# Kernel tuning notes

Hardware: AMD Instinct MI355X
Metric: run time of the kernel (lower is better)

The kernel has to match this reference:

```python
import jax, jax.numpy as jnp
import numpy as np

B, T, D, E, TOP_K = 8, 2048, 512, 8, 2


def setup_inputs() -> dict:
    key = jax.random.key(0)
    ks = jax.random.split(key, 8)
    s = 0.02
    return {
        "x": jax.random.normal(ks[0], (B, T, D), dtype=jnp.float32),
        "eps": jax.random.normal(ks[1], (B, T, E), dtype=jnp.float32),
        "Wr": jax.random.normal(ks[2], (D, E), dtype=jnp.float32) * s,
        "br": jnp.zeros((E,), dtype=jnp.float32),
        "Wn": jax.random.normal(ks[3], (D, E), dtype=jnp.float32) * s,
        "bn": jnp.zeros((E,), dtype=jnp.float32),
        "Wk": jax.random.normal(ks[4], (E, D, D), dtype=jnp.float32) * s,
        "bk": jnp.zeros((E, D), dtype=jnp.float32),
    }


def reference(x, eps, Wr, br, Wn, bn, Wk, bk):
    # Noisy top-k router (NoisyTopkRouter.forward)
    logits = jnp.einsum("btd,de->bte", x, Wr) + br            # [B,T,E]
    noise_logits = jnp.einsum("btd,de->bte", x, Wn) + bn      # [B,T,E]
    noisy = logits + eps * jax.nn.softplus(noise_logits)      # [B,T,E]
    _, top_idx = jax.lax.top_k(noisy, TOP_K)                  # [B,T,k]
    # mask[b,t,e] = True iff expert e is in the token's top-k
    topk_mask = jax.nn.one_hot(top_idx, E, dtype=jnp.float32).sum(-2) > 0
    sparse_logits = jnp.where(topk_mask, noisy, -jnp.inf)
    gating = jax.nn.softmax(sparse_logits, axis=-1)           # zero for non-top-k experts
    # Dense dispatch: every expert's Linear applied to all tokens, then
    # gating (zero outside top-k) selects/scales — same math as the masked
    # gather + per-expert Linear + gating scale in SparseMoE.forward.
    expert_out = jnp.einsum("btd,edh->bteh", x, Wk) + bk      # [B,T,E,D]
    out = jnp.einsum("bte,bteh->bth", gating, expert_out)     # [B,T,D]
    return out
```

## Files before the change

kernel.cpp:

```cpp
#include <hip/hip_runtime.h>
#include <hip/hip_bf16.h>
#include <math.h>

#define B_    8
#define T_    2048
#define NTOK  (B_ * T_)
#define D_    512
#define E_    8
#define CAP   NTOK

#define RV_TOK    16
#define RV_THR    256
#define XS_STRIDE 132
#define WS_FLOATS 2108

typedef __attribute__((ext_vector_type(4))) float f32x4;
typedef __attribute__((ext_vector_type(8))) short short8;

__device__ __forceinline__ void async_load16(const void* g, void* l) {
    __builtin_amdgcn_global_load_lds(
        (const __attribute__((address_space(1))) unsigned int*)g,
        (__attribute__((address_space(3))) unsigned int*)l,
        16, 0, 0);
}

__global__ __launch_bounds__(256) void transpose_wk(
    const float* __restrict__ Wk, __hip_bfloat16* __restrict__ Wkt)
{
    __shared__ float tile[32][33];
    const int e  = blockIdx.z;
    const int d0 = blockIdx.x * 32;
    const int h0 = blockIdx.y * 32;
    const int tx = threadIdx.x, ty = threadIdx.y;

    const float* src = Wk + ((size_t)e * D_ + d0) * D_ + h0;
    #pragma unroll
    for (int r = ty; r < 32; r += 8)
        tile[r][tx] = src[(size_t)r * D_ + tx];
    __syncthreads();
    __hip_bfloat16* dst = Wkt + ((size_t)e * D_ + h0) * D_ + d0;
    #pragma unroll
    for (int r = ty; r < 32; r += 8)
        dst[(size_t)r * D_ + tx] = __float2bfloat16(tile[tx][r]);
}

__global__ __launch_bounds__(RV_THR) void router_kernel(
    const float* __restrict__ x,
    const float* __restrict__ eps,
    const float* __restrict__ Wr,
    const float* __restrict__ br,
    const float* __restrict__ Wn,
    const float* __restrict__ bn,
    __hip_bfloat16* __restrict__ xb,
    uint4* __restrict__ top2)
{
    __shared__ float xs[RV_TOK * XS_STRIDE];
    __shared__ float wsh[WS_FLOATS];

    const int tid  = threadIdx.x;
    const int tok0 = blockIdx.x * RV_TOK;
    const int lane = tid & 63, wv = tid >> 6;
    const int kidx = lane >> 2, ts = lane & 3;
    const int tl = wv * 4 + ts;
    const int wk = tid >> 1, wh = tid & 1;

    float acc[16];
    #pragma unroll
    for (int c = 0; c < 16; ++c) acc[c] = 0.f;

    for (int kc = 0; kc < D_; kc += 128) {
        #pragma unroll
        for (int it = 0; it < 2; ++it) {
            const int f   = it * RV_THR + tid;
            const int row = f >> 5, col = (f & 31) * 4;
            const f32x4 v = *(const f32x4*)(x + (size_t)(tok0 + row) * D_ + kc + col);
            *(f32x4*)(xs + row * XS_STRIDE + col) = v;
            union { __hip_bfloat16 h[4]; uint2 u; } cv;
            cv.h[0] = __float2bfloat16(v.x); cv.h[1] = __float2bfloat16(v.y);
            cv.h[2] = __float2bfloat16(v.z); cv.h[3] = __float2bfloat16(v.w);
            *(uint2*)(xb + (size_t)(tok0 + row) * D_ + kc + col) = cv.u;
        }
        {
            const float* src = (wh ? Wn : Wr) + (size_t)(kc + wk) * E_;
            const f32x4 w0 = *(const f32x4*)(src);
            const f32x4 w1 = *(const f32x4*)(src + 4);
            float* dst = wsh + wk * 16 + (wk >> 3) * 4 + wh * 8;
            *(f32x4*)(dst)     = w0;
            *(f32x4*)(dst + 4) = w1;
        }
        __syncthreads();

        const float* xra = xs + tl * XS_STRIDE + kidx * 8;
        const f32x4 xa0 = *(const f32x4*)(xra);
        const f32x4 xa1 = *(const f32x4*)(xra + 4);
        const float* wbase = wsh + kidx * 132;
        #pragma unroll
        for (int kk = 0; kk < 8; ++kk) {
            const float xav = (kk < 4) ? xa0[kk] : xa1[kk - 4];
            const float* wrow = wbase + kk * 16;
            #pragma unroll
            for (int c4 = 0; c4 < 4; ++c4) {
                const f32x4 w = *(const f32x4*)(wrow + c4 * 4);
                #pragma unroll
                for (int c = 0; c < 4; ++c)
                    acc[c4 * 4 + c] = fmaf(xav, w[c], acc[c4 * 4 + c]);
            }
        }
        __syncthreads();
    }

    #pragma unroll
    for (int off = 4; off < 64; off <<= 1) {
        #pragma unroll
        for (int c = 0; c < 16; ++c)
            acc[c] += __shfl_xor(acc[c], off);
    }

    if (lane < 4) {
        const int tok = tok0 + tl;
        float nv[8];
        #pragma unroll
        for (int e = 0; e < 8; ++e) {
            const float nl = acc[8 + e] + bn[e];
            const float sp = fmaxf(nl, 0.f) + log1pf(expf(-fabsf(nl)));
            nv[e] = acc[e] + br[e] + eps[(size_t)tok * E_ + e] * sp;
        }
        int i1 = 0; float v1 = nv[0];
        #pragma unroll
        for (int e = 1; e < 8; ++e)
            if (nv[e] > v1) { v1 = nv[e]; i1 = e; }
        int i2 = -1; float v2 = -3.4e38f;
        #pragma unroll
        for (int e = 0; e < 8; ++e)
            if (e != i1 && nv[e] > v2) { v2 = nv[e]; i2 = e; }
        const float t  = expf(v2 - v1);
        const float g1 = 1.f / (1.f + t);
        const float g2 = t / (1.f + t);
        top2[tok] = make_uint4((unsigned)i1 | ((unsigned)i2 << 8),
                               __float_as_uint(g1), __float_as_uint(g2), 0u);
    }
}

__global__ __launch_bounds__(256) void bucket_kernel(
    const uint4* __restrict__ top2,
    int* __restrict__ counts,
    uint2* __restrict__ entries)
{
    __shared__ int hist[E_];
    __shared__ int base[E_];
    const int tid = threadIdx.x;
    const int tok = blockIdx.x * 256 + tid;
    if (tid < E_) hist[tid] = 0;
    __syncthreads();
    const uint4 t = top2[tok];
    const int i1 = t.x & 0xff, i2 = (t.x >> 8) & 0xff;
    const int l1 = atomicAdd(&hist[i1], 1);
    const int l2 = atomicAdd(&hist[i2], 1);
    __syncthreads();
    if (tid < E_) base[tid] = atomicAdd(counts + tid, hist[tid]);
    __syncthreads();
    entries[(size_t)i1 * CAP + base[i1] + l1] = make_uint2((unsigned)tok, t.y);
    entries[(size_t)i2 * CAP + base[i2] + l2] =
        make_uint2((unsigned)tok | 0x80000000u, t.z);
}

__global__ __launch_bounds__(256, 2) void moe_gemm(
    const __hip_bfloat16* __restrict__ xb,
    const __hip_bfloat16* __restrict__ wkt,
    const float* __restrict__ bk,
    const int* __restrict__ counts,
    const uint2* __restrict__ entries,
    __hip_bfloat16* __restrict__ outg,
    float* __restrict__ out,
    int use_slots)
{
    constexpr int BM = 128, BN = 256, BK = 32;
    __shared__ __hip_bfloat16 As[BM * BK];
    __shared__ __hip_bfloat16 Bs[BN * BK];
    __shared__ uint2 ent[BM];

    const int e  = blockIdx.z;
    const int mt = blockIdx.y;
    const int nt = blockIdx.x;
    const int cnt = counts[e];
    if (mt * BM >= cnt) return;

    const int tid = threadIdx.x;
    const int wave = tid >> 6, lane = tid & 63;

    if (tid < BM) {
        const int idx = mt * BM + tid;
        ent[tid] = (idx < cnt) ? entries[(size_t)e * CAP + idx] : make_uint2(0u, 0u);
    }
    __syncthreads();

    const int quad = lane >> 4, lr = lane & 15;
    const int wm = wave >> 1, wn = wave & 1;
    const int sub = lane >> 2, part = lane & 3;

    f32x4 acc[4][8];
    #pragma unroll
    for (int i = 0; i < 4; ++i)
        #pragma unroll
        for (int j = 0; j < 8; ++j) acc[i][j] = (f32x4){0.f, 0.f, 0.f, 0.f};

    const size_t tok0 = ent[wave * 32 + sub].x & 0x7fffffffu;
    const size_t tok1 = ent[wave * 32 + 16 + sub].x & 0x7fffffffu;
    const size_t brow0 = (size_t)e * D_ + nt * BN + wave * 64 + sub;

    for (int k0 = 0; k0 < D_; k0 += BK) {
        async_load16(xb + tok0 * D_ + k0 + part * 8, As + (wave * 32) * BK);
        async_load16(xb + tok1 * D_ + k0 + part * 8, As + (wave * 32 + 16) * BK);
        #pragma unroll
        for (int q = 0; q < 4; ++q)
            async_load16(wkt + (brow0 + q * 16) * D_ + k0 + part * 8,
                         Bs + (wave * 64 + q * 16) * BK);
        __syncthreads();

        short8 a[4], b[8];
        #pragma unroll
        for (int i = 0; i < 4; ++i)
            a[i] = *(const short8*)(As + (wm * 64 + i * 16 + lr) * BK + quad * 8);
        #pragma unroll
        for (int j = 0; j < 8; ++j)
            b[j] = *(const short8*)(Bs + (wn * 128 + j * 16 + lr) * BK + quad * 8);
        #pragma unroll
        for (int i = 0; i < 4; ++i)
            #pragma unroll
            for (int j = 0; j < 8; ++j)
                acc[i][j] = __builtin_amdgcn_mfma_f32_16x16x32_bf16(a[i], b[j], acc[i][j], 0, 0, 0);
        __syncthreads();
    }

    const int colbase = nt * BN + wn * 128 + lr;
    float bkv[8];
    #pragma unroll
    for (int j = 0; j < 8; ++j) bkv[j] = bk[e * D_ + colbase + j * 16];

    #pragma unroll
    for (int i = 0; i < 4; ++i) {
        #pragma unroll
        for (int r = 0; r < 4; ++r) {
            const int row = wm * 64 + i * 16 + quad * 4 + r;
            if (mt * BM + row < cnt) {
                const uint2 en = ent[row];
                const unsigned ts2 = en.x;
                const float g = __uint_as_float(en.y);
                if (use_slots) {
                    __hip_bfloat16* orow = outg + ((size_t)(ts2 >> 31) * NTOK
                                          + (ts2 & 0x7fffffffu)) * D_ + colbase;
                    #pragma unroll
                    for (int j = 0; j < 8; ++j)
                        orow[j * 16] = __float2bfloat16(g * (acc[i][j][r] + bkv[j]));
                } else {
                    float* orow = out + (size_t)(ts2 & 0x7fffffffu) * D_ + colbase;
                    #pragma unroll
                    for (int j = 0; j < 8; ++j)
                        atomicAdd(orow + j * 16, g * (acc[i][j][r] + bkv[j]));
                }
            }
        }
    }
}

__global__ __launch_bounds__(256) void combine_kernel(
    const __hip_bfloat16* __restrict__ outg, float* __restrict__ out)
{
    const size_t i = ((size_t)blockIdx.x * 256 + threadIdx.x) * 8;
    const uint4 u0 = *(const uint4*)(outg + i);
    const uint4 u1 = *(const uint4*)(outg + (size_t)NTOK * D_ + i);
    const unsigned* a = (const unsigned*)&u0;
    const unsigned* b = (const unsigned*)&u1;
    float o[8];
    #pragma unroll
    for (int k = 0; k < 4; ++k) {
        o[2*k]   = __uint_as_float(a[k] << 16) + __uint_as_float(b[k] << 16);
        o[2*k+1] = __uint_as_float(a[k] & 0xffff0000u)
                 + __uint_as_float(b[k] & 0xffff0000u);
    }
    *(f32x4*)(out + i)     = *(f32x4*)(o);
    *(f32x4*)(out + i + 4) = *(f32x4*)(o + 4);
}

extern "C" void kernel_launch(void* const* d_in, const int* in_sizes, int n_in,
                              void* d_out, int out_size, void* d_ws, size_t ws_size,
                              hipStream_t stream) {
    const float* x   = (const float*)d_in[0];
    const float* eps = (const float*)d_in[1];
    const float* Wr  = (const float*)d_in[2];
    const float* br  = (const float*)d_in[3];
    const float* Wn  = (const float*)d_in[4];
    const float* bn  = (const float*)d_in[5];
    const float* Wk  = (const float*)d_in[6];
    const float* bk  = (const float*)d_in[7];
    float* out = (float*)d_out;

    char* ws = (char*)d_ws;
    size_t off = 0;
    int* counts = (int*)(ws + off);                     off += 256;
    uint2* entries = (uint2*)(ws + off);                off += (size_t)E_ * CAP * 8;
    __hip_bfloat16* xb = (__hip_bfloat16*)(ws + off);   off += (size_t)NTOK * D_ * 2;
    __hip_bfloat16* wkt = (__hip_bfloat16*)(ws + off);  off += (size_t)E_ * D_ * D_ * 2;
    uint4* top2 = (uint4*)(ws + off);                   off += (size_t)NTOK * 16;
    __hip_bfloat16* outg = (__hip_bfloat16*)(ws + off); off += (size_t)2 * NTOK * D_ * 2;
    const int use_slots = (ws_size >= off) ? 1 : 0;

    hipMemsetAsync(counts, 0, E_ * sizeof(int), stream);
    if (!use_slots)
        hipMemsetAsync(out, 0, (size_t)out_size * sizeof(float), stream);

    transpose_wk<<<dim3(16, 16, E_), dim3(32, 8), 0, stream>>>(Wk, wkt);
    router_kernel<<<dim3(NTOK / RV_TOK), dim3(RV_THR), 0, stream>>>(
        x, eps, Wr, br, Wn, bn, xb, top2);
    bucket_kernel<<<dim3(NTOK / 256), dim3(256), 0, stream>>>(top2, counts, entries);
    moe_gemm<<<dim3(D_ / 256, CAP / 128, E_), dim3(256), 0, stream>>>(
        xb, wkt, bk, counts, entries, outg, out, use_slots);
    if (use_slots)
        combine_kernel<<<dim3((NTOK * D_) / (256 * 8)), dim3(256), 0, stream>>>(outg, out);
}
```

Baseline: 177.0 us.

## Bucket tokens by expert pair and compute both experts in one GEMM tile

Tokens are grouped by their unordered pair of top-2 experts (28 buckets), so each GEMM block computes both expert outputs for its tokens and writes the gated sum directly to the fp32 output. This removes the bf16 per-slot intermediate buffer, the combine kernel, and the atomic/memset fallback path, and each token's activation tile is loaded once instead of twice. In exchange there are 28 buckets, so partial tiles add padding waste, the grid grows to 28 in z with many early-exiting blocks, and each block streams two weight tiles with a narrower BN.

Measured after the change: 168.5 us. 4.8% less time.

```diff
diff --git a/kernel.cpp b/kernel.cpp
--- a/kernel.cpp
+++ b/kernel.cpp
@@ -7,6 +7,7 @@
 #define NTOK  (B_ * T_)
 #define D_    512
 #define E_    8
+#define NPAIR 28
 #define CAP   NTOK
 
 #define RV_TOK    16
@@ -144,24 +145,25 @@
 __global__ __launch_bounds__(256) void bucket_kernel(
     const uint4* __restrict__ top2,
     int* __restrict__ counts,
-    uint2* __restrict__ entries)
+    uint4* __restrict__ entries)
 {
-    __shared__ int hist[E_];
-    __shared__ int base[E_];
+    __shared__ int hist[NPAIR];
+    __shared__ int base[NPAIR];
     const int tid = threadIdx.x;
     const int tok = blockIdx.x * 256 + tid;
-    if (tid < E_) hist[tid] = 0;
+    if (tid < NPAIR) hist[tid] = 0;
     __syncthreads();
     const uint4 t = top2[tok];
     const int i1 = t.x & 0xff, i2 = (t.x >> 8) & 0xff;
-    const int l1 = atomicAdd(&hist[i1], 1);
-    const int l2 = atomicAdd(&hist[i2], 1);
-    __syncthreads();
-    if (tid < E_) base[tid] = atomicAdd(counts + tid, hist[tid]);
-    __syncthreads();
-    entries[(size_t)i1 * CAP + base[i1] + l1] = make_uint2((unsigned)tok, t.y);
-    entries[(size_t)i2 * CAP + base[i2] + l2] =
-        make_uint2((unsigned)tok | 0x80000000u, t.z);
+    const int a = min(i1, i2), b = max(i1, i2);
+    const unsigned ga = (i1 < i2) ? t.y : t.z;
+    const unsigned gb = (i1 < i2) ? t.z : t.y;
+    const int p = a * (15 - a) / 2 + (b - a - 1);
+    const int l = atomicAdd(&hist[p], 1);
+    __syncthreads();
+    if (tid < NPAIR) base[tid] = atomicAdd(counts + tid, hist[tid]);
+    __syncthreads();
+    entries[(size_t)p * CAP + base[p] + l] = make_uint4((unsigned)tok, ga, gb, 0u);
 }
 
 __global__ __launch_bounds__(256, 2) void moe_gemm(
@@ -169,28 +171,31 @@
     const __hip_bfloat16* __restrict__ wkt,
     const float* __restrict__ bk,
     const int* __restrict__ counts,
-    const uint2* __restrict__ entries,
-    __hip_bfloat16* __restrict__ outg,
-    float* __restrict__ out,
-    int use_slots)
+    const uint4* __restrict__ entries,
+    float* __restrict__ out)
 {
-    constexpr int BM = 128, BN = 256, BK = 32;
+    constexpr int BM = 128, BN = 128, BK = 32;
     __shared__ __hip_bfloat16 As[BM * BK];
-    __shared__ __hip_bfloat16 Bs[BN * BK];
-    __shared__ uint2 ent[BM];
-
-    const int e  = blockIdx.z;
+    __shared__ __hip_bfloat16 Bs[2][BN * BK];
+    __shared__ uint4 ent[BM];
+
+    const int p  = blockIdx.z;
     const int mt = blockIdx.y;
     const int nt = blockIdx.x;
-    const int cnt = counts[e];
+    const int cnt = counts[p];
     if (mt * BM >= cnt) return;
+
+    int e1 = 0, rem = p;
+    while (rem >= 7 - e1) { rem -= 7 - e1; ++e1; }
+    const int e2 = e1 + 1 + rem;
 
     const int tid = threadIdx.x;
     const int wave = tid >> 6, lane = tid & 63;
 
     if (tid < BM) {
         const int idx = mt * BM + tid;
-        ent[tid] = (idx < cnt) ? entries[(size_t)e * CAP + idx] : make_uint2(0u, 0u);
+        ent[tid] = (idx < cnt) ? entries[(size_t)p * CAP + idx]
+                               : make_uint4(0u, 0u, 0u, 0u);
     }
     __syncthreads();
 
@@ -198,44 +203,55 @@
     const int wm = wave >> 1, wn = wave & 1;
     const int sub = lane >> 2, part = lane & 3;
 
-    f32x4 acc[4][8];
+    f32x4 accA[4][4], accB[4][4];
     #pragma unroll
     for (int i = 0; i < 4; ++i)
         #pragma unroll
-        for (int j = 0; j < 8; ++j) acc[i][j] = (f32x4){0.f, 0.f, 0.f, 0.f};
-
-    const size_t tok0 = ent[wave * 32 + sub].x & 0x7fffffffu;
-    const size_t tok1 = ent[wave * 32 + 16 + sub].x & 0x7fffffffu;
-    const size_t brow0 = (size_t)e * D_ + nt * BN + wave * 64 + sub;
+        for (int j = 0; j < 4; ++j) {
+            accA[i][j] = (f32x4){0.f, 0.f, 0.f, 0.f};
+            accB[i][j] = (f32x4){0.f, 0.f, 0.f, 0.f};
+        }
+
+    const size_t tok0 = ent[wave * 32 + sub].x;
+    const size_t tok1 = ent[wave * 32 + 16 + sub].x;
+    const size_t brow1 = (size_t)e1 * D_ + nt * BN + wave * 32 + sub;
+    const size_t brow2 = (size_t)e2 * D_ + nt * BN + wave * 32 + sub;
 
     for (int k0 = 0; k0 < D_; k0 += BK) {
         async_load16(xb + tok0 * D_ + k0 + part * 8, As + (wave * 32) * BK);
         async_load16(xb + tok1 * D_ + k0 + part * 8, As + (wave * 32 + 16) * BK);
-        #pragma unroll
-        for (int q = 0; q < 4; ++q)
-            async_load16(wkt + (brow0 + q * 16) * D_ + k0 + part * 8,
-                         Bs + (wave * 64 + q * 16) * BK);
+        async_load16(wkt + brow1 * D_ + k0 + part * 8, Bs[0] + (wave * 32) * BK);
+        async_load16(wkt + (brow1 + 16) * D_ + k0 + part * 8, Bs[0] + (wave * 32 + 16) * BK);
+        async_load16(wkt + brow2 * D_ + k0 + part * 8, Bs[1] + (wave * 32) * BK);
+        async_load16(wkt + (brow2 + 16) * D_ + k0 + part * 8, Bs[1] + (wave * 32 + 16) * BK);
         __syncthreads();
 
-        short8 a[4], b[8];
+        short8 a[4], b1[4], b2[4];
         #pragma unroll
         for (int i = 0; i < 4; ++i)
             a[i] = *(const short8*)(As + (wm * 64 + i * 16 + lr) * BK + quad * 8);
         #pragma unroll
-        for (int j = 0; j < 8; ++j)
-            b[j] = *(const short8*)(Bs + (wn * 128 + j * 16 + lr) * BK + quad * 8);
+        for (int j = 0; j < 4; ++j) {
+            b1[j] = *(const short8*)(Bs[0] + (wn * 64 + j * 16 + lr) * BK + quad * 8);
+            b2[j] = *(const short8*)(Bs[1] + (wn * 64 + j * 16 + lr) * BK + quad * 8);
+        }
         #pragma unroll
         for (int i = 0; i < 4; ++i)
             #pragma unroll
-            for (int j = 0; j < 8; ++j)
-                acc[i][j] = __builtin_amdgcn_mfma_f32_16x16x32_bf16(a[i], b[j], acc[i][j], 0, 0, 0);
+            for (int j = 0; j < 4; ++j) {
+                accA[i][j] = __builtin_amdgcn_mfma_f32_16x16x32_bf16(a[i], b1[j], accA[i][j], 0, 0, 0);
+                accB[i][j] = __builtin_amdgcn_mfma_f32_16x16x32_bf16(a[i], b2[j], accB[i][j], 0, 0, 0);
+            }
         __syncthreads();
     }
 
-    const int colbase = nt * BN + wn * 128 + lr;
-    float bkv[8];
-    #pragma unroll
-    for (int j = 0; j < 8; ++j) bkv[j] = bk[e * D_ + colbase + j * 16];
+    const int colbase = nt * BN + wn * 64 + lr;
+    float bkA[4], bkB[4];
+    #pragma unroll
+    for (int j = 0; j < 4; ++j) {
+        bkA[j] = bk[e1 * D_ + colbase + j * 16];
+        bkB[j] = bk[e2 * D_ + colbase + j * 16];
+    }
 
     #pragma unroll
     for (int i = 0; i < 4; ++i) {
@@ -243,43 +259,17 @@
         for (int r = 0; r < 4; ++r) {
             const int row = wm * 64 + i * 16 + quad * 4 + r;
             if (mt * BM + row < cnt) {
-                const uint2 en = ent[row];
-                const unsigned ts2 = en.x;
-                const float g = __uint_as_float(en.y);
-                if (use_slots) {
-                    __hip_bfloat16* orow = outg + ((size_t)(ts2 >> 31) * NTOK
-                                          + (ts2 & 0x7fffffffu)) * D_ + colbase;
-                    #pragma unroll
-                    for (int j = 0; j < 8; ++j)
-                        orow[j * 16] = __float2bfloat16(g * (acc[i][j][r] + bkv[j]));
-                } else {
-                    float* orow = out + (size_t)(ts2 & 0x7fffffffu) * D_ + colbase;
-                    #pragma unroll
-                    for (int j = 0; j < 8; ++j)
-                        atomicAdd(orow + j * 16, g * (acc[i][j][r] + bkv[j]));
-                }
+                const uint4 en = ent[row];
+                const float ga = __uint_as_float(en.y);
+                const float gb = __uint_as_float(en.z);
+                float* orow = out + (size_t)en.x * D_ + colbase;
+                #pragma unroll
+                for (int j = 0; j < 4; ++j)
+                    orow[j * 16] = ga * (accA[i][j][r] + bkA[j])
+                                 + gb * (accB[i][j][r] + bkB[j]);
             }
         }
     }
-}
-
-__global__ __launch_bounds__(256) void combine_kernel(
-    const __hip_bfloat16* __restrict__ outg, float* __restrict__ out)
-{
-    const size_t i = ((size_t)blockIdx.x * 256 + threadIdx.x) * 8;
-    const uint4 u0 = *(const uint4*)(outg + i);
-    const uint4 u1 = *(const uint4*)(outg + (size_t)NTOK * D_ + i);
-    const unsigned* a = (const unsigned*)&u0;
-    const unsigned* b = (const unsigned*)&u1;
-    float o[8];
-    #pragma unroll
-    for (int k = 0; k < 4; ++k) {
-        o[2*k]   = __uint_as_float(a[k] << 16) + __uint_as_float(b[k] << 16);
-        o[2*k+1] = __uint_as_float(a[k] & 0xffff0000u)
-                 + __uint_as_float(b[k] & 0xffff0000u);
-    }
-    *(f32x4*)(out + i)     = *(f32x4*)(o);
-    *(f32x4*)(out + i + 4) = *(f32x4*)(o + 4);
 }
 
 extern "C" void kernel_launch(void* const* d_in, const int* in_sizes, int n_in,
@@ -298,23 +288,18 @@
     char* ws = (char*)d_ws;
     size_t off = 0;
     int* counts = (int*)(ws + off);                     off += 256;
-    uint2* entries = (uint2*)(ws + off);                off += (size_t)E_ * CAP * 8;
+    uint4* entries = (uint4*)(ws + off);                off += (size_t)NPAIR * CAP * 16;
     __hip_bfloat16* xb = (__hip_bfloat16*)(ws + off);   off += (size_t)NTOK * D_ * 2;
     __hip_bfloat16* wkt = (__hip_bfloat16*)(ws + off);  off += (size_t)E_ * D_ * D_ * 2;
     uint4* top2 = (uint4*)(ws + off);                   off += (size_t)NTOK * 16;
-    __hip_bfloat16* outg = (__hip_bfloat16*)(ws + off); off += (size_t)2 * NTOK * D_ * 2;
-    const int use_slots = (ws_size >= off) ? 1 : 0;
-
-    hipMemsetAsync(counts, 0, E_ * sizeof(int), stream);
-    if (!use_slots)
-        hipMemsetAsync(out, 0, (size_t)out_size * sizeof(float), stream);
+    (void)ws_size;
+
+    hipMemsetAsync(counts, 0, NPAIR * sizeof(int), stream);
 
     transpose_wk<<<dim3(16, 16, E_), dim3(32, 8), 0, stream>>>(Wk, wkt);
     router_kernel<<<dim3(NTOK / RV_TOK), dim3(RV_THR), 0, stream>>>(
         x, eps, Wr, br, Wn, bn, xb, top2);
     bucket_kernel<<<dim3(NTOK / 256), dim3(256), 0, stream>>>(top2, counts, entries);
-    moe_gemm<<<dim3(D_ / 256, CAP / 128, E_), dim3(256), 0, stream>>>(
-        xb, wkt, bk, counts, entries, outg, out, use_slots);
-    if (use_slots)
-        combine_kernel<<<dim3((NTOK * D_) / (256 * 8)), dim3(256), 0, stream>>>(outg, out);
-}
+    moe_gemm<<<dim3(D_ / 128, CAP / 128, NPAIR), dim3(256), 0, stream>>>(
+        xb, wkt, bk, counts, entries, out);
+}
```
